# Kernel optimization log

Measured on AMD Instinct MI355X. Metric: run time of the kernel, lower is better.

The kernel has to match this reference:

```python
import jax, jax.numpy as jnp
from jax import lax
import numpy as np

B, T, C = 32, 2048, 512
CLAMP_LO, CLAMP_HI = 1e-4, 1.0 - 1e-4


def setup_inputs() -> dict:
    key = jax.random.key(0)
    x = jax.random.normal(key, (B, T, C), dtype=jnp.float32)
    # parameter initialized at logit(0.9), repeated per channel
    logit_alpha = jnp.full((C,), float(np.log(0.9 / 0.1)), dtype=jnp.float32)
    delta = jnp.asarray(1.0, dtype=jnp.float32)
    return {"x": x, "logit_alpha": logit_alpha, "delta": delta}


def reference(x, logit_alpha, delta):
    # x: [B, T, C]; logit_alpha: [C]; delta: scalar
    a = jnp.clip(jax.nn.sigmoid(logit_alpha), CLAMP_LO, CLAMP_HI).astype(x.dtype)  # [C]
    one_minus_a = 1.0 - a  # [C], broadcasts over [B, C]
    d = delta.astype(x.dtype)

    def step(y_prev, x_t):  # y_prev, x_t: [B, C]
        r = x_t - y_prev
        g = jnp.where(jnp.abs(r) <= d, r, d * jnp.sign(r))  # Huber gradient
        y = y_prev + one_minus_a * g
        return y, y

    y0 = x[:, 0, :]  # [B, C]
    xs = jnp.swapaxes(x[:, 1:, :], 0, 1)  # [T-1, B, C]
    _, ys = lax.scan(step, y0, xs)  # ys: [T-1, B, C]
    y = jnp.concatenate([y0[None], ys], axis=0)  # [T, B, C]
    return jnp.swapaxes(y, 0, 1)  # [B, T, C]
```

## Files before the change

### kernel.cpp

```cpp
#include <hip/hip_runtime.h>
#include <math.h>


#define TT 2048
#define CCH 512
#define NBATCH 32
#define UNR 64
#define NB (TT / UNR)

template<bool RELOAD>
__device__ __forceinline__ void consume_block(float (&buf)[UNR], int kblk,
                                              float& yv, float oma, float d,
                                              const float* __restrict__ xp,
                                              float* __restrict__ yp)
{
    const size_t tb = (size_t)kblk * UNR;
    #pragma unroll
    for (int i = 0; i < UNR; ++i) {
        float r = buf[i] - yv;
        if (RELOAD)
            buf[i] = __builtin_nontemporal_load(
                         xp + (tb + (size_t)(2 * UNR + i)) * CCH);
        yv += oma * fminf(fmaxf(r, -d), d);
        __builtin_nontemporal_store(yv, yp + (tb + (size_t)i) * CCH);
    }
}

__global__ __launch_bounds__(64, 1)
void huber_ema_kernel(const float* __restrict__ x,
                      const float* __restrict__ logit_alpha,
                      const float* __restrict__ delta,
                      float* __restrict__ y)
{
    const int blk = blockIdx.x;
    const int b   = blk >> 3;
    const int cc  = blk & 7;
    const int c   = (cc << 6) + threadIdx.x;

    const float la = logit_alpha[c];
    float a = 1.0f / (1.0f + expf(-la));
    a = fminf(fmaxf(a, 1e-4f), 1.0f - 1e-4f);
    const float oma = 1.0f - a;
    const float d = delta[0];

    const size_t base = ((size_t)b * TT) * CCH + (size_t)c;
    const float* __restrict__ xp = x + base;
    float*       __restrict__ yp = y + base;

    float bufA[UNR], bufB[UNR];

    #pragma unroll
    for (int i = 0; i < UNR; ++i)
        bufA[i] = __builtin_nontemporal_load(xp + (size_t)i * CCH);
    #pragma unroll
    for (int i = 0; i < UNR; ++i)
        bufB[i] = __builtin_nontemporal_load(xp + (size_t)(UNR + i) * CCH);

    float yv = bufA[0];
    bufA[0] = __builtin_nontemporal_load(xp + (size_t)(2 * UNR) * CCH);
    __builtin_nontemporal_store(yv, yp);
    #pragma unroll
    for (int i = 1; i < UNR; ++i) {
        float r = bufA[i] - yv;
        bufA[i] = __builtin_nontemporal_load(xp + (size_t)(2 * UNR + i) * CCH);
        yv += oma * fminf(fmaxf(r, -d), d);
        __builtin_nontemporal_store(yv, yp + (size_t)i * CCH);
    }

    for (int k = 1; k + 3 < NB; k += 2) {
        consume_block<true>(bufB, k,     yv, oma, d, xp, yp);
        consume_block<true>(bufA, k + 1, yv, oma, d, xp, yp);
    }
    consume_block<true >(bufB, NB - 3, yv, oma, d, xp, yp);
    consume_block<false>(bufA, NB - 2, yv, oma, d, xp, yp);
    consume_block<false>(bufB, NB - 1, yv, oma, d, xp, yp);
}

extern "C" void kernel_launch(void* const* d_in, const int* in_sizes, int n_in,
                              void* d_out, int out_size, void* d_ws, size_t ws_size,
                              hipStream_t stream) {
    const float* x  = (const float*)d_in[0];
    const float* la = (const float*)d_in[1];
    const float* dl = (const float*)d_in[2];
    float* y = (float*)d_out;

    const int n_blocks = NBATCH * (CCH / 64);
    huber_ema_kernel<<<dim3(n_blocks), dim3(64), 0, stream>>>(x, la, dl, y);
}
```

Measured before the change: 232.2 us.

## Stage input tiles through LDS with float4 loads and double buffering

Input is now loaded as float4 vectors, with each lane covering 4 channels across 16 time steps, then transposed through a double-buffered LDS tile so each lane reads back its own channel sequentially. Fewer, wider global load instructions should raise the bytes in flight per wave for this latency-bound single-wave-per-block scan. The cost is extra LDS write and read traffic and register pressure from 16 float4 prefetch registers. There are no barriers, which is safe only because each block is one 64-lane wavefront. Stores are now ordinary rather than nontemporal.

Result: slower. 264.1 us (+13.7%).

```diff
diff --git a/kernel.cpp b/kernel.cpp
--- a/kernel.cpp
+++ b/kernel.cpp
@@ -2,29 +2,10 @@
 #include <math.h>
 
 
-#define TT 2048
-#define CCH 512
-#define NBATCH 32
-#define UNR 64
-#define NB (TT / UNR)
-
-template<bool RELOAD>
-__device__ __forceinline__ void consume_block(float (&buf)[UNR], int kblk,
-                                              float& yv, float oma, float d,
-                                              const float* __restrict__ xp,
-                                              float* __restrict__ yp)
-{
-    const size_t tb = (size_t)kblk * UNR;
-    #pragma unroll
-    for (int i = 0; i < UNR; ++i) {
-        float r = buf[i] - yv;
-        if (RELOAD)
-            buf[i] = __builtin_nontemporal_load(
-                         xp + (tb + (size_t)(2 * UNR + i)) * CCH);
-        yv += oma * fminf(fmaxf(r, -d), d);
-        __builtin_nontemporal_store(yv, yp + (tb + (size_t)i) * CCH);
-    }
-}
+#define TT   2048
+#define CC   512
+#define TILE 64
+#define NTIL (TT / TILE)
 
 __global__ __launch_bounds__(64, 1)
 void huber_ema_kernel(const float* __restrict__ x,
@@ -32,48 +13,69 @@
                       const float* __restrict__ delta,
                       float* __restrict__ y)
 {
-    const int blk = blockIdx.x;
-    const int b   = blk >> 3;
-    const int cc  = blk & 7;
-    const int c   = (cc << 6) + threadIdx.x;
+    const int blk  = blockIdx.x;
+    const int b    = blk >> 3;
+    const int cc   = blk & 7;
+    const int lane = threadIdx.x;
 
-    const float la = logit_alpha[c];
+    const int chc = (cc << 6) + lane;
+    const float la = logit_alpha[chc];
     float a = 1.0f / (1.0f + expf(-la));
     a = fminf(fmaxf(a, 1e-4f), 1.0f - 1e-4f);
     const float oma = 1.0f - a;
     const float d = delta[0];
 
-    const size_t base = ((size_t)b * TT) * CCH + (size_t)c;
-    const float* __restrict__ xp = x + base;
-    float*       __restrict__ yp = y + base;
+    const float* __restrict__ xb = x + (size_t)b * TT * CC + (cc << 6);
+    float*       __restrict__ yb = y + (size_t)b * TT * CC + (cc << 6);
 
-    float bufA[UNR], bufB[UNR];
+    const int tl = lane >> 4;
+    const int c4 = (lane & 15) << 2;
+    const float* __restrict__ xl = xb + (size_t)tl * CC + c4;
+
+    __shared__ float lds[2][TILE * 64];
+
+    float4 xr[16];
+    float  xin[TILE];
+
+    float yv = xb[lane];
 
     #pragma unroll
-    for (int i = 0; i < UNR; ++i)
-        bufA[i] = __builtin_nontemporal_load(xp + (size_t)i * CCH);
+    for (int g = 0; g < 16; ++g)
+        xr[g] = *(const float4*)(xl + (size_t)(g * 4) * CC);
     #pragma unroll
-    for (int i = 0; i < UNR; ++i)
-        bufB[i] = __builtin_nontemporal_load(xp + (size_t)(UNR + i) * CCH);
+    for (int g = 0; g < 16; ++g)
+        *(float4*)&lds[0][g * 256 + (lane << 2)] = xr[g];
+    #pragma unroll
+    for (int g = 0; g < 16; ++g)
+        xr[g] = *(const float4*)(xl + (size_t)(TILE + g * 4) * CC);
 
-    float yv = bufA[0];
-    bufA[0] = __builtin_nontemporal_load(xp + (size_t)(2 * UNR) * CCH);
-    __builtin_nontemporal_store(yv, yp);
-    #pragma unroll
-    for (int i = 1; i < UNR; ++i) {
-        float r = bufA[i] - yv;
-        bufA[i] = __builtin_nontemporal_load(xp + (size_t)(2 * UNR + i) * CCH);
-        yv += oma * fminf(fmaxf(r, -d), d);
-        __builtin_nontemporal_store(yv, yp + (size_t)i * CCH);
+    for (int k = 0; k < NTIL; ++k) {
+        float* __restrict__ buf  = lds[k & 1];
+        float* __restrict__ bufn = lds[(k + 1) & 1];
+
+        if (k + 1 < NTIL) {
+            #pragma unroll
+            for (int g = 0; g < 16; ++g)
+                *(float4*)&bufn[g * 256 + (lane << 2)] = xr[g];
+        }
+        if (k + 2 < NTIL) {
+            #pragma unroll
+            for (int g = 0; g < 16; ++g)
+                xr[g] = *(const float4*)(xl + (size_t)((k + 2) * TILE + g * 4) * CC);
+        }
+
+        #pragma unroll
+        for (int i = 0; i < TILE; ++i)
+            xin[i] = buf[i * 64 + lane];
+
+        const size_t tb = (size_t)k * TILE;
+        #pragma unroll
+        for (int i = 0; i < TILE; ++i) {
+            float r = xin[i] - yv;
+            yv += oma * fminf(fmaxf(r, -d), d);
+            yb[(tb + (size_t)i) * CC + lane] = yv;
+        }
     }
-
-    for (int k = 1; k + 3 < NB; k += 2) {
-        consume_block<true>(bufB, k,     yv, oma, d, xp, yp);
-        consume_block<true>(bufA, k + 1, yv, oma, d, xp, yp);
-    }
-    consume_block<true >(bufB, NB - 3, yv, oma, d, xp, yp);
-    consume_block<false>(bufA, NB - 2, yv, oma, d, xp, yp);
-    consume_block<false>(bufB, NB - 1, yv, oma, d, xp, yp);
 }
 
 extern "C" void kernel_launch(void* const* d_in, const int* in_sizes, int n_in,
@@ -84,6 +86,5 @@
     const float* dl = (const float*)d_in[2];
     float* y = (float*)d_out;
 
-    const int n_blocks = NBATCH * (CCH / 64);
-    huber_ema_kernel<<<dim3(n_blocks), dim3(64), 0, stream>>>(x, la, dl, y);
+    huber_ema_kernel<<<dim3(256), dim3(64), 0, stream>>>(x, la, dl, y);
 }
```
